# Kernel optimization log

Hardware: AMD Instinct MI355X
Metric: run time of the kernel (lower is better)

Reference implementation:

```python
import jax, jax.numpy as jnp
import numpy as np

NUM_HEAD = 8   # in_channels // 64 for in_channels=512
DIM = 8        # per-head dim (== num_head in this module)
H_CH = NUM_HEAD * DIM  # 64
SCALE = DIM ** (-0.5)


def _conv(x, w, b, padding):
    # x: [N,C,H,W], w: [O,I,kh,kw]
    out = jax.lax.conv_general_dilated(
        x, w, window_strides=(1, 1), padding=padding,
        dimension_numbers=("NCHW", "OIHW", "NCHW"))
    return out + b[None, :, None, None]


def setup_inputs() -> dict:
    key = jax.random.key(0)
    ks = jax.random.split(key, 4)
    N, C, H, W = 4, 512, 48, 48
    x = jax.random.normal(ks[0], (N, C, H, W), dtype=jnp.float32)
    qkv_w = jax.random.normal(ks[1], (3 * H_CH, C, 1, 1), dtype=jnp.float32) * 0.05
    qkv_b = jnp.zeros((3 * H_CH,), dtype=jnp.float32)
    pos_w = jax.random.normal(ks[2], (H_CH, H_CH, 3, 3), dtype=jnp.float32) * 0.05
    pos_b = jnp.zeros((H_CH,), dtype=jnp.float32)
    res_w = jax.random.normal(ks[3], (C, H_CH, 1, 1), dtype=jnp.float32) * 0.05
    res_b = jnp.zeros((C,), dtype=jnp.float32)
    return {"x": x, "qkv_w": qkv_w, "qkv_b": qkv_b,
            "pos_w": pos_w, "pos_b": pos_b,
            "res_w": res_w, "res_b": res_b}


def reference(x, qkv_w, qkv_b, pos_w, pos_b, res_w, res_b):
    N, C, H, W = x.shape
    L = H * W
    # 1x1 conv QKV projection -> [N, 3h, H, W]
    qkv = _conv(x, qkv_w, qkv_b, "VALID")
    # [N, num_head, 3*dim, L]
    qkv = qkv.reshape(N, NUM_HEAD, 3 * DIM, L)
    q, k, v = qkv[:, :, :DIM], qkv[:, :, DIM:2 * DIM], qkv[:, :, 2 * DIM:]
    # attn = q^T @ k * scale : [N, nh, L, L], softmax over keys (last dim)
    attn = jnp.einsum("nhdq,nhdk->nhqk", q, k) * SCALE
    attn = jax.nn.softmax(attn, axis=-1)
    # out = v @ attn^T : [N, nh, dim, L]
    out = jnp.einsum("nhdk,nhqk->nhdq", v, attn)
    out = out.reshape(N, H_CH, H, W)
    # positional branch: 3x3 conv on v
    pos = _conv(v.reshape(N, H_CH, H, W), pos_w, pos_b, "SAME")
    out = out + pos
    # resume 1x1 conv -> [N, out_channels, H, W]
    return _conv(out, res_w, res_b, "VALID")
```

## Files before the change

kernel.cpp:

```cpp
#include <hip/hip_runtime.h>

#define L_ATT 2304
#define QSCALE_LOG2E 0.5100695712f

using bh8 = __attribute__((ext_vector_type(8))) short;
using f4  = __attribute__((ext_vector_type(4))) float;

#if __has_builtin(__builtin_amdgcn_exp2f)
#define EXP2(x) __builtin_amdgcn_exp2f(x)
#else
#define EXP2(x) exp2f(x)
#endif

__device__ inline short f2b(float f) {
    union { float f; unsigned u; } c; c.f = f;
    unsigned r = (c.u + 0x7FFFu + ((c.u >> 16) & 1u)) >> 16;
    return (short)r;
}
__device__ inline float b2f(short s) {
    union { unsigned u; float f; } c;
    c.u = ((unsigned)(unsigned short)s) << 16;
    return c.f;
}
__device__ inline int packhi(float lo, float hi) {
    return (int)__builtin_amdgcn_perm(__float_as_uint(hi), __float_as_uint(lo), 0x07060302u);
}

__global__ __launch_bounds__(256) void prep_kernel(
    const float* __restrict__ x, const float* __restrict__ qkv_w,
    const float* __restrict__ res_w, const float* __restrict__ pos_w,
    short* __restrict__ xt, short* __restrict__ wqb,
    short* __restrict__ reswb, short* __restrict__ wqp)
{
    __shared__ float s[64][68];
    const int g = blockIdx.x;
    if (g < 272) {
        int j = g * 256 + threadIdx.x;
        if (j < 24576) {
            float4 v = ((const float4*)qkv_w)[j];
            short4 o = { f2b(v.x), f2b(v.y), f2b(v.z), f2b(v.w) };
            *(short4*)(wqb + (size_t)j * 4) = o;
        } else if (j < 32768) {
            int idx = j - 24576;
            float4 v = ((const float4*)res_w)[idx];
            short4 o = { f2b(v.x), f2b(v.y), f2b(v.z), f2b(v.w) };
            *(short4*)(reswb + (size_t)idx * 4) = o;
        } else {
            int e = j - 32768;
            wqp[e] = f2b(pos_w[(size_t)(e & 4095) * 9 + (e >> 12)]);
        }
        return;
    }
    const int gg = g - 272;
    const int l0 = (gg % 36) * 64, k0 = ((gg / 36) & 7) * 64, n = gg / 288;
    const int tr = threadIdx.x >> 4, tc4 = (threadIdx.x & 15) * 4;
    const float* xp = x + ((size_t)n * 512 + k0) * L_ATT + l0;
#pragma unroll
    for (int r = 0; r < 4; ++r)
        *(float4*)&s[tr + r * 16][tc4] =
            *(const float4*)(xp + (size_t)(tr + r * 16) * L_ATT + tc4);
    __syncthreads();
    short* op = xt + ((size_t)n * L_ATT + l0) * 512 + k0;
#pragma unroll
    for (int r = 0; r < 4; ++r) {
        int l = tr + r * 16;
        short4 o = { f2b(s[tc4 + 0][l]), f2b(s[tc4 + 1][l]),
                     f2b(s[tc4 + 2][l]), f2b(s[tc4 + 3][l]) };
        *(short4*)(op + (size_t)l * 512 + tc4) = o;
    }
}

__global__ __launch_bounds__(256) void qkv_kernel(
    const short* __restrict__ xt, const short* __restrict__ wqb,
    const float* __restrict__ qkv_b, short* __restrict__ qt8,
    short* __restrict__ kt8, short* __restrict__ vt, short* __restrict__ vle)
{
    const int g = blockIdx.x;
    const int xcd = g & 7, rr = g >> 3;
    const int y = rr % 3, grp = rr / 3;
    const int code = grp * 8 + xcd;
    const int l0 = (code % 72) * 32, oc0 = y * 64, n = code / 72;

    const int lane = threadIdx.x & 63, wave = threadIdx.x >> 6;
    const int col = lane & 15, quad = lane >> 4;
    const int ocb = oc0 + wave * 16;

    f4 acc[2];
    acc[0] = (f4){0.f, 0.f, 0.f, 0.f};
    acc[1] = (f4){0.f, 0.f, 0.f, 0.f};

    const short* arow = wqb + (size_t)(ocb + col) * 512 + quad * 8;
    const short* brow = xt + ((size_t)n * L_ATT + l0 + col) * 512 + quad * 8;

#pragma unroll 4
    for (int k0 = 0; k0 < 512; k0 += 32) {
        bh8 af = *(const bh8*)(arow + k0);
        bh8 b0 = *(const bh8*)(brow + k0);
        bh8 b1 = *(const bh8*)(brow + (size_t)16 * 512 + k0);
        acc[0] = __builtin_amdgcn_mfma_f32_16x16x32_bf16(af, b0, acc[0], 0, 0, 0);
        acc[1] = __builtin_amdgcn_mfma_f32_16x16x32_bf16(af, b1, acc[1], 0, 0, 0);
    }

    const int obase = ocb + quad * 4;
    const int h = obase / 24;
    const int r0 = obase - h * 24;
    const int slice = n * 8 + h;

#pragma unroll
    for (int nt = 0; nt < 2; ++nt) {
        int l = l0 + nt * 16 + col;
        float v[4];
#pragma unroll
        for (int reg = 0; reg < 4; ++reg) v[reg] = acc[nt][reg] + qkv_b[obase + reg];
        if (r0 < 8) {
            short4 o = { f2b(v[0] * QSCALE_LOG2E), f2b(v[1] * QSCALE_LOG2E),
                         f2b(v[2] * QSCALE_LOG2E), f2b(v[3] * QSCALE_LOG2E) };
            *(short4*)(qt8 + ((size_t)slice * L_ATT + l) * 8 + r0) = o;
        } else if (r0 < 16) {
            short4 o = { f2b(v[0]), f2b(v[1]), f2b(v[2]), f2b(v[3]) };
            *(short4*)(kt8 + ((size_t)slice * L_ATT + l) * 8 + (r0 - 8)) = o;
        } else {
            short4 o = { f2b(v[0]), f2b(v[1]), f2b(v[2]), f2b(v[3]) };
            int d0 = r0 - 16;
#pragma unroll
            for (int reg = 0; reg < 4; ++reg)
                vt[((size_t)slice * 8 + d0 + reg) * L_ATT + l] = ((short*)&o)[reg];
            *(short4*)(vle + ((size_t)n * L_ATT + l) * 64 + h * 8 + d0) = o;
        }
    }
}

__global__ __launch_bounds__(256) void attnpos_kernel(
    const short* __restrict__ qt8, const short* __restrict__ kt8,
    const short* __restrict__ vt, const short* __restrict__ vle,
    const short* __restrict__ wqp, const float* __restrict__ pbias,
    float* __restrict__ att, short* __restrict__ pcv)
{
    __shared__ short smem[4112];
    const int g = blockIdx.x;
    const int tid = threadIdx.x;
    const int lane = tid & 63, wave = tid >> 6;
    const int col = lane & 15, quad = lane >> 4;

    if (g < 1152) {
        const int h = g & 7, r = g >> 3;
        const int n = r / 36, qt = r % 36;
        const int q0 = qt * 64;
        const int slice = n * 8 + h;

        const short* qs  = qt8 + (size_t)slice * L_ATT * 8;
        const short* ks8 = kt8 + (size_t)slice * L_ATT * 8;
        const short* vb  = vt  + (size_t)slice * 8 * L_ATT;

        if (tid < 16) smem[4096 + tid] = (tid < 8) ? (short)0x3F80 : (short)0;

        bh8 zero8 = {0, 0, 0, 0, 0, 0, 0, 0};
        bh8 qf = zero8;
        if (quad == 0)
            qf = *(const bh8*)(qs + (size_t)(q0 + wave * 16 + col) * 8);

        int kidx[4];
#pragma unroll
        for (int nt = 0; nt < 4; ++nt)
            kidx[nt] = (quad == 0) ? (nt * 16 + col) * 8 : 4104;
        int vidx[2];
#pragma unroll
        for (int ks = 0; ks < 2; ++ks)
            vidx[ks] = (col < 8)
                     ? col * 64 + ((ks * 32 + quad * 8 + col * 8) & 63)
                     : ((col == 8) ? 4096 : 4104);

        const int ksl = ((lane >> 5) & 1) * 32 + ((lane >> 2) & 1) * 16
                      + ((lane >> 3) & 3) * 4 + (lane & 3);
        const int vd = lane >> 3, vkc = (lane & 7) * 8;
        const int vsl = vd * 64 + ((vkc + vd * 8) & 63);

        if (wave == 0) {
            *(uint4*)&smem[ksl * 8]       = *(const uint4*)(ks8 + (size_t)lane * 8);
            *(uint4*)&smem[512 + ksl * 8] = *(const uint4*)(ks8 + (size_t)(64 + lane) * 8);
        } else if (wave == 1) {
            *(uint4*)&smem[2048 + vsl]       = *(const uint4*)(vb + (size_t)vd * L_ATT + vkc);
            *(uint4*)&smem[2048 + 512 + vsl] = *(const uint4*)(vb + (size_t)vd * L_ATT + 64 + vkc);
        }
        __syncthreads();

        f4 oacc = (f4){0.f, 0.f, 0.f, 0.f};
        int p = 0;
        for (int t = 0; t < 18; ++t) {
            uint4 dk0, dk1, dv0, dv1;
            if (wave == 0) {
                dk0 = *(const uint4*)(ks8 + (size_t)((t * 2 + 2) * 64 + lane) * 8);
                dk1 = *(const uint4*)(ks8 + (size_t)((t * 2 + 3) * 64 + lane) * 8);
            } else if (wave == 1) {
                dv0 = *(const uint4*)(vb + (size_t)vd * L_ATT + (t * 2 + 2) * 64 + vkc);
                dv1 = *(const uint4*)(vb + (size_t)vd * L_ATT + (t * 2 + 3) * 64 + vkc);
            }

#pragma unroll
            for (int u = 0; u < 2; ++u) {
                const int ku = (quad == 0) ? p * 1024 + u * 512 : 0;
                const int vu = (col < 8) ? 2048 + p * 1024 + u * 512 : 0;
                bh8 kf[4], vf[2];
#pragma unroll
                for (int nt = 0; nt < 4; ++nt) kf[nt] = *(const bh8*)&smem[kidx[nt] + ku];
#pragma unroll
                for (int ks = 0; ks < 2; ++ks) vf[ks] = *(const bh8*)&smem[vidx[ks] + vu];

                f4 s[4];
#pragma unroll
                for (int nt = 0; nt < 4; ++nt) {
                    f4 z = (f4){0.f, 0.f, 0.f, 0.f};
                    s[nt] = __builtin_amdgcn_mfma_f32_16x16x32_bf16(kf[nt], qf, z, 0, 0, 0);
                }
                float e[4][4];
#pragma unroll
                for (int nt = 0; nt < 4; ++nt)
#pragma unroll
                    for (int reg = 0; reg < 4; ++reg)
                        e[nt][reg] = EXP2(s[nt][reg]);
#pragma unroll
                for (int ks = 0; ks < 2; ++ks) {
                    union { int i[4]; bh8 v; } pu;
                    pu.i[0] = packhi(e[2 * ks][0],     e[2 * ks][1]);
                    pu.i[1] = packhi(e[2 * ks][2],     e[2 * ks][3]);
                    pu.i[2] = packhi(e[2 * ks + 1][0], e[2 * ks + 1][1]);
                    pu.i[3] = packhi(e[2 * ks + 1][2], e[2 * ks + 1][3]);
                    oacc = __builtin_amdgcn_mfma_f32_16x16x32_bf16(vf[ks], pu.v, oacc, 0, 0, 0);
                }
            }

            if (wave == 0) {
                *(uint4*)&smem[(p ^ 1) * 1024 + ksl * 8]       = dk0;
                *(uint4*)&smem[(p ^ 1) * 1024 + 512 + ksl * 8] = dk1;
            } else if (wave == 1) {
                *(uint4*)&smem[2048 + (p ^ 1) * 1024 + vsl]       = dv0;
                *(uint4*)&smem[2048 + (p ^ 1) * 1024 + 512 + vsl] = dv1;
            }
            p ^= 1;
            __syncthreads();
        }

        float ls  = __shfl(oacc[0], 32 + col);
        float inv = 1.0f / ls;
        if (quad < 2) {
            int q = q0 + wave * 16 + col;
            float4 o = { oacc[0] * inv, oacc[1] * inv,
                         oacc[2] * inv, oacc[3] * inv };
            *(float4*)(att + ((size_t)n * L_ATT + q) * 64 + h * 8 + quad * 4) = o;
        }
        return;
    }

    const int gf = g - 1152;
    const int l0 = (gf % 144) * 16, n = gf / 144;
    const int t = wave;

    const int la = l0 + col;
    const int ya = la / 48, xa = la - ya * 48;

    f4 acc = (f4){0.f, 0.f, 0.f, 0.f};
    const short* vbase = vle + (size_t)n * L_ATT * 64;

#pragma unroll
    for (int q = 0; q < 9; ++q) {
        const int dy = q / 3 - 1, dx = q - (q / 3) * 3 - 1;
        const bool valid = ((unsigned)(ya + dy) < 48u) && ((unsigned)(xa + dx) < 48u);
        const short* ap = vbase + (size_t)(la + dy * 48 + dx) * 64 + quad * 8;
#pragma unroll
        for (int ks = 0; ks < 2; ++ks) {
            bh8 af = {0, 0, 0, 0, 0, 0, 0, 0};
            if (valid) af = *(const bh8*)(ap + ks * 32);
            bh8 bf = *(const bh8*)(wqp + ((size_t)q * 64 + t * 16 + col) * 64
                                   + ks * 32 + quad * 8);
            acc = __builtin_amdgcn_mfma_f32_16x16x32_bf16(af, bf, acc, 0, 0, 0);
        }
    }

    short* op = pcv + (size_t)n * L_ATT * 64;
    const int oc = t * 16 + col;
    const float bb = pbias[oc];
#pragma unroll
    for (int reg = 0; reg < 4; ++reg) {
        int l = l0 + quad * 4 + reg;
        op[(size_t)l * 64 + oc] = f2b(acc[reg] + bb);
    }
}

__global__ __launch_bounds__(256) void res_kernel(
    const float* __restrict__ att, const short* __restrict__ pcv,
    const short* __restrict__ reswb, const float* __restrict__ res_b,
    float* __restrict__ out)
{
    const int g = blockIdx.x;
    const int xcd = g & 7, rr = g >> 3;
    const int y = rr & 7, grp = rr >> 3;
    const int code = grp * 8 + xcd;
    const int l0 = (code % 36) * 64, oc0 = y * 64, n = code / 36;

    const int lane = threadIdx.x & 63, wave = threadIdx.x >> 6;
    const int col = lane & 15, quad = lane >> 4;
    const int ocb = oc0 + wave * 16;

    f4 acc[4];
#pragma unroll
    for (int nt = 0; nt < 4; ++nt) acc[nt] = (f4){0.f, 0.f, 0.f, 0.f};

#pragma unroll
    for (int ks = 0; ks < 2; ++ks) {
        bh8 af = *(const bh8*)(reswb + (size_t)(ocb + col) * 64 + ks * 32 + quad * 8);
        const int ch = ks * 32 + quad * 8;
#pragma unroll
        for (int nt = 0; nt < 4; ++nt) {
            const int l = l0 + nt * 16 + col;
            const float* ab = att + ((size_t)n * L_ATT + l) * 64 + ch;
            float4 a0 = *(const float4*)ab;
            float4 a1 = *(const float4*)(ab + 4);
            bh8 pv = *(const bh8*)(pcv + ((size_t)n * L_ATT + l) * 64 + ch);
            union { int i[4]; bh8 v; } pu;
            pu.i[0] = packhi(a0.x + b2f(pv[0]), a0.y + b2f(pv[1]));
            pu.i[1] = packhi(a0.z + b2f(pv[2]), a0.w + b2f(pv[3]));
            pu.i[2] = packhi(a1.x + b2f(pv[4]), a1.y + b2f(pv[5]));
            pu.i[3] = packhi(a1.z + b2f(pv[6]), a1.w + b2f(pv[7]));
            acc[nt] = __builtin_amdgcn_mfma_f32_16x16x32_bf16(af, pu.v, acc[nt], 0, 0, 0);
        }
    }

#pragma unroll
    for (int nt = 0; nt < 4; ++nt) {
        int l = l0 + nt * 16 + col;
#pragma unroll
        for (int reg = 0; reg < 4; ++reg) {
            int oc = ocb + quad * 4 + reg;
            out[((size_t)n * 512 + oc) * L_ATT + l] = acc[nt][reg] + res_b[oc];
        }
    }
}

extern "C" void kernel_launch(void* const* d_in, const int* in_sizes, int n_in,
                              void* d_out, int out_size, void* d_ws, size_t ws_size,
                              hipStream_t stream)
{
    const float* x      = (const float*)d_in[0];
    const float* qkv_w  = (const float*)d_in[1];
    const float* qkv_b  = (const float*)d_in[2];
    const float* pos_w  = (const float*)d_in[3];
    const float* pos_b  = (const float*)d_in[4];
    const float* res_w  = (const float*)d_in[5];
    const float* res_b  = (const float*)d_in[6];
    float* out = (float*)d_out;

    char* ws = (char*)d_ws;
    short* xt    = (short*)(ws);
    float* att   = (float*)(ws);
    short* qt8   = (short*)(ws + 9437184);
    short* kt8   = (short*)(ws + 10616832);
    short* vt    = (short*)(ws + 11796480);
    short* pcv   = (short*)(ws + 12976128);
    short* wqb   = (short*)(ws + 14155776);
    short* reswb = (short*)(ws + 14352384);
    short* vle   = (short*)(ws + 14417920);
    short* wqp   = (short*)(ws + 15597568);

    prep_kernel<<<1424, 256, 0, stream>>>(x, qkv_w, res_w, pos_w, xt, wqb, reswb, wqp);
    qkv_kernel<<<864, 256, 0, stream>>>(xt, wqb, qkv_b, qt8, kt8, vt, vle);
    attnpos_kernel<<<1728, 256, 0, stream>>>(qt8, kt8, vt, vle, wqp, pos_b, att, pcv);
    res_kernel<<<1152, 256, 0, stream>>>(att, pcv, reswb, res_b, out);
}
```

Baseline: 156.6 us.

## Double attention block size to 512 threads with 128 queries per block

```diff
diff --git a/kernel.cpp b/kernel.cpp
--- a/kernel.cpp
+++ b/kernel.cpp
@@ -130,7 +130,7 @@
     }
 }
 
-__global__ __launch_bounds__(256) void attnpos_kernel(
+__global__ __launch_bounds__(512) void attnpos_kernel(
     const short* __restrict__ qt8, const short* __restrict__ kt8,
     const short* __restrict__ vt, const short* __restrict__ vle,
     const short* __restrict__ wqp, const float* __restrict__ pbias,
@@ -142,10 +142,10 @@
     const int lane = tid & 63, wave = tid >> 6;
     const int col = lane & 15, quad = lane >> 4;
 
-    if (g < 1152) {
+    if (g < 576) {
         const int h = g & 7, r = g >> 3;
-        const int n = r / 36, qt = r % 36;
-        const int q0 = qt * 64;
+        const int n = r / 18, qt = r % 18;
+        const int q0 = qt * 128;
         const int slice = n * 8 + h;
 
         const short* qs  = qt8 + (size_t)slice * L_ATT * 8;
@@ -175,26 +175,22 @@
         const int vd = lane >> 3, vkc = (lane & 7) * 8;
         const int vsl = vd * 64 + ((vkc + vd * 8) & 63);
 
-        if (wave == 0) {
-            *(uint4*)&smem[ksl * 8]       = *(const uint4*)(ks8 + (size_t)lane * 8);
-            *(uint4*)&smem[512 + ksl * 8] = *(const uint4*)(ks8 + (size_t)(64 + lane) * 8);
-        } else if (wave == 1) {
-            *(uint4*)&smem[2048 + vsl]       = *(const uint4*)(vb + (size_t)vd * L_ATT + vkc);
-            *(uint4*)&smem[2048 + 512 + vsl] = *(const uint4*)(vb + (size_t)vd * L_ATT + 64 + vkc);
-        }
+        if (wave < 2)
+            *(uint4*)&smem[wave * 512 + ksl * 8] =
+                *(const uint4*)(ks8 + (size_t)(wave * 64 + lane) * 8);
+        else if (wave < 4)
+            *(uint4*)&smem[2048 + (wave - 2) * 512 + vsl] =
+                *(const uint4*)(vb + (size_t)vd * L_ATT + (wave - 2) * 64 + vkc);
         __syncthreads();
 
         f4 oacc = (f4){0.f, 0.f, 0.f, 0.f};
         int p = 0;
         for (int t = 0; t < 18; ++t) {
-            uint4 dk0, dk1, dv0, dv1;
-            if (wave == 0) {
-                dk0 = *(const uint4*)(ks8 + (size_t)((t * 2 + 2) * 64 + lane) * 8);
-                dk1 = *(const uint4*)(ks8 + (size_t)((t * 2 + 3) * 64 + lane) * 8);
-            } else if (wave == 1) {
-                dv0 = *(const uint4*)(vb + (size_t)vd * L_ATT + (t * 2 + 2) * 64 + vkc);
-                dv1 = *(const uint4*)(vb + (size_t)vd * L_ATT + (t * 2 + 3) * 64 + vkc);
-            }
+            uint4 dst;
+            if (wave < 2)
+                dst = *(const uint4*)(ks8 + (size_t)((t * 2 + 2 + wave) * 64 + lane) * 8);
+            else if (wave < 4)
+                dst = *(const uint4*)(vb + (size_t)vd * L_ATT + (t * 2 + wave) * 64 + vkc);
 
 #pragma unroll
             for (int u = 0; u < 2; ++u) {
@@ -229,13 +225,10 @@
                 }
             }
 
-            if (wave == 0) {
-                *(uint4*)&smem[(p ^ 1) * 1024 + ksl * 8]       = dk0;
-                *(uint4*)&smem[(p ^ 1) * 1024 + 512 + ksl * 8] = dk1;
-            } else if (wave == 1) {
-                *(uint4*)&smem[2048 + (p ^ 1) * 1024 + vsl]       = dv0;
-                *(uint4*)&smem[2048 + (p ^ 1) * 1024 + 512 + vsl] = dv1;
-            }
+            if (wave < 2)
+                *(uint4*)&smem[(p ^ 1) * 1024 + wave * 512 + ksl * 8] = dst;
+            else if (wave < 4)
+                *(uint4*)&smem[2048 + (p ^ 1) * 1024 + (wave - 2) * 512 + vsl] = dst;
             p ^= 1;
             __syncthreads();
         }
@@ -251,11 +244,11 @@
         return;
     }
 
-    const int gf = g - 1152;
-    const int l0 = (gf % 144) * 16, n = gf / 144;
-    const int t = wave;
-
-    const int la = l0 + col;
+    const int gf = g - 576;
+    const int l0 = (gf % 72) * 32, n = gf / 72;
+    const int t = wave & 3, lh = wave >> 2;
+
+    const int la = l0 + lh * 16 + col;
     const int ya = la / 48, xa = la - ya * 48;
 
     f4 acc = (f4){0.f, 0.f, 0.f, 0.f};
@@ -281,7 +274,7 @@
     const float bb = pbias[oc];
 #pragma unroll
     for (int reg = 0; reg < 4; ++reg) {
-        int l = l0 + quad * 4 + reg;
+        int l = l0 + lh * 16 + quad * 4 + reg;
         op[(size_t)l * 64 + oc] = f2b(acc[reg] + bb);
     }
 }
@@ -363,6 +356,6 @@
 
     prep_kernel<<<1424, 256, 0, stream>>>(x, qkv_w, res_w, pos_w, xt, wqb, reswb, wqp);
     qkv_kernel<<<864, 256, 0, stream>>>(xt, wqb, qkv_b, qt8, kt8, vt, vle);
-    attnpos_kernel<<<1728, 256, 0, stream>>>(qt8, kt8, vt, vle, wqp, pos_b, att, pcv);
+    attnpos_kernel<<<864, 512, 0, stream>>>(qt8, kt8, vt, vle, wqp, pos_b, att, pcv);
     res_kernel<<<1152, 256, 0, stream>>>(att, pcv, reswb, res_b, out);
 }
```

Result: no change. 155.7 us (-0.6%).
